# Kernel tuning notes

Measured on AMD Instinct MI355X. Metric: run time of the kernel, lower is better.

The kernel has to match this reference:

```python
import jax, jax.numpy as jnp
import numpy as np

NUM_TYPES = 4  # unique atom types, e.g. H,C,N,O
N_DESC = 384   # descriptor width (nDescriptors())


def setup_inputs() -> dict:
    key = jax.random.key(0)
    k1, k2, k3 = jax.random.split(key, 3)
    n_confs, n_atoms = 2048, 64
    coords = jax.random.normal(k1, (n_confs, n_atoms, 3), dtype=jnp.float32)
    atom_types = jax.random.randint(k2, (n_confs, n_atoms), 0, NUM_TYPES, dtype=jnp.int64)
    W = jax.random.normal(k3, (3, N_DESC), dtype=jnp.float32)
    return {"coords": coords, "atom_types": atom_types, "W": W}


def reference(coords, atom_types, W):
    n_confs, n_atoms, _ = coords.shape
    # stub descriptor computer: per-atom descriptor, (n_confs*n_atoms, N_DESC)
    desc = jnp.tanh(coords.reshape(-1, 3) @ W)
    at2type = atom_types.reshape(-1)                      # (N,)
    # conformer index for every atom: [0,0,...,0,1,1,...]
    at2conf = jnp.repeat(jnp.arange(n_confs, dtype=jnp.int64), n_atoms)
    # stable sort by atom type (routing permutation)
    perm = jnp.argsort(at2type, stable=True)              # (N,)
    desc_sorted = desc[perm]                              # gather (N, N_DESC)
    at2conf_sorted = at2conf[perm]                        # (N,)
    at_type_count = jnp.bincount(at2type, length=NUM_TYPES)  # split sizes per type
    # per-type buckets = desc_sorted split at cumsum(at_type_count); returned
    # concatenated with counts to keep shapes static under jit.
    return desc_sorted, at2conf_sorted, at_type_count
```

## Files before the change

kernel.cpp:

```cpp
#include <hip/hip_runtime.h>

#define NDESC 384
#define NTYPES 4
#define BLOCK_ATOMS 256
#define NTHREADS 384

typedef unsigned int uint32;
typedef unsigned long long u64;
typedef float f4 __attribute__((ext_vector_type(4)));

__device__ __forceinline__ float fast_tanh(float x) {
  float e = __builtin_amdgcn_exp2f(x * 2.8853900817779268f);
  return 1.0f - 2.0f * __builtin_amdgcn_rcpf(1.0f + e);
}

__global__ __launch_bounds__(BLOCK_ATOMS) void hist_kernel(
    const int* __restrict__ types, uint32* __restrict__ blockHist, int n) {
  __shared__ uint32 waveCnt[BLOCK_ATOMS / 64][NTYPES];
  int tid = threadIdx.x;
  int idx = blockIdx.x * BLOCK_ATOMS + tid;
  int ty = (idx < n) ? types[idx] : -1;
  int wave = tid >> 6, lane = tid & 63;
  for (int t = 0; t < NTYPES; ++t) {
    u64 m = __ballot(ty == t);
    if (lane == 0) waveCnt[wave][t] = (uint32)__popcll(m);
  }
  __syncthreads();
  if (tid < NTYPES) {
    uint32 s = 0;
    for (int w = 0; w < BLOCK_ATOMS / 64; ++w) s += waveCnt[w][tid];
    blockHist[blockIdx.x * NTYPES + tid] = s;
  }
}

__global__ __launch_bounds__(NTHREADS, 6) void main_kernel(
    const float* __restrict__ coords, const int* __restrict__ types,
    const float* __restrict__ W, const uint32* __restrict__ blockHist,
    float* __restrict__ descOut, float* __restrict__ confOut,
    float* __restrict__ countsOut, int n, int nb) {
  __shared__ float sC[BLOCK_ATOMS][3];
  __shared__ f4 sRankData[BLOCK_ATOMS];
  __shared__ uint32 waveCnt[BLOCK_ATOMS / 64][NTYPES];
  __shared__ uint32 sTot[NTYPES];
  __shared__ uint32 sOff[NTYPES];
  __shared__ uint32 sCum[NTYPES];

  int tid = threadIdx.x;
  int bid = blockIdx.x;
  int base = bid * BLOCK_ATOMS;

  int r = tid / 96;
  int c = tid - r * 96;
  int d0 = 4 * c;

  f4 W0 = *reinterpret_cast<const f4*>(W + d0);
  f4 W1 = *reinterpret_cast<const f4*>(W + NDESC + d0);
  f4 W2 = *reinterpret_cast<const f4*>(W + 2 * NDESC + d0);

  for (int i = tid; i < BLOCK_ATOMS * 3; i += NTHREADS) {
    int g = base * 3 + i;
    sC[i / 3][i % 3] = (g < n * 3) ? coords[g] : 0.0f;
  }

  int idx = base + tid;
  int ty = -1;
  if (tid < BLOCK_ATOMS && idx < n) ty = types[idx];
  int wave = tid >> 6, lane = tid & 63;
  int myrank = 0;
  if (tid < BLOCK_ATOMS) {
    for (int t = 0; t < NTYPES; ++t) {
      u64 m = __ballot(ty == t);
      if (lane == 0) waveCnt[wave][t] = (uint32)__popcll(m);
      if (t == ty) myrank = (int)__popcll(m & ((1ull << lane) - 1ull));
    }
  }

  if (wave < NTYPES) {
    int t = wave;
    uint32 tot = 0, pre = 0;
    for (int b = lane; b < nb; b += 64) {
      uint32 h = blockHist[b * NTYPES + t];
      tot += h;
      if (b < bid) pre += h;
    }
    for (int off = 32; off > 0; off >>= 1) {
      tot += __shfl_down(tot, off);
      pre += __shfl_down(pre, off);
    }
    if (lane == 0) { sTot[t] = tot; sOff[t] = pre; }
  }
  __syncthreads();
  if (tid == 0) {
    uint32 b = 0, cc = 0;
    for (int t = 0; t < NTYPES; ++t) {
      sOff[t] += b;
      b += sTot[t];
      uint32 cnt = 0;
      for (int w = 0; w < BLOCK_ATOMS / 64; ++w) cnt += waveCnt[w][t];
      sCum[t] = cc;
      cc += cnt;
    }
  }
  if (bid == 0 && tid < NTYPES) countsOut[tid] = (float)sTot[tid];
  __syncthreads();

  if (tid < BLOCK_ATOMS && ty >= 0) {
    uint32 fullrank = (uint32)myrank;
    for (int w = 0; w < wave; ++w) fullrank += waveCnt[w][ty];
    uint32 pos = sOff[ty] + fullrank;
    uint32 brk = sCum[ty] + fullrank;
    f4 rd;
    rd.x = sC[tid][0];
    rd.y = sC[tid][1];
    rd.z = sC[tid][2];
    rd.w = __uint_as_float(pos);
    sRankData[brk] = rd;
    confOut[pos] = (float)(idx >> 6);
  }
  __syncthreads();

  int valid = n - base;
  if (valid > BLOCK_ATOMS) valid = BLOCK_ATOMS;

  if (valid == BLOCK_ATOMS) {
#pragma unroll 4
    for (int k0 = 0; k0 < BLOCK_ATOMS; k0 += 4) {
      int k = k0 + r;
      f4 rd = sRankData[k];
      uint32 pos = __float_as_uint(rd.w);
      f4 v;
      v.x = fast_tanh(rd.x * W0.x + rd.y * W1.x + rd.z * W2.x);
      v.y = fast_tanh(rd.x * W0.y + rd.y * W1.y + rd.z * W2.y);
      v.z = fast_tanh(rd.x * W0.z + rd.y * W1.z + rd.z * W2.z);
      v.w = fast_tanh(rd.x * W0.w + rd.y * W1.w + rd.z * W2.w);
      *reinterpret_cast<f4*>(descOut + (size_t)pos * NDESC + d0) = v;
    }
  } else {
    for (int k0 = 0; k0 < BLOCK_ATOMS; k0 += 4) {
      int k = k0 + r;
      if (k < valid) {
        f4 rd = sRankData[k];
        uint32 pos = __float_as_uint(rd.w);
        f4 v;
        v.x = fast_tanh(rd.x * W0.x + rd.y * W1.x + rd.z * W2.x);
        v.y = fast_tanh(rd.x * W0.y + rd.y * W1.y + rd.z * W2.y);
        v.z = fast_tanh(rd.x * W0.z + rd.y * W1.z + rd.z * W2.z);
        v.w = fast_tanh(rd.x * W0.w + rd.y * W1.w + rd.z * W2.w);
        *reinterpret_cast<f4*>(descOut + (size_t)pos * NDESC + d0) = v;
      }
    }
  }
}

extern "C" void kernel_launch(void* const* d_in, const int* in_sizes, int n_in,
                              void* d_out, int out_size, void* d_ws, size_t ws_size,
                              hipStream_t stream) {
  const float* coords = (const float*)d_in[0];
  const int* types = (const int*)d_in[1];
  const float* W = (const float*)d_in[2];

  int n = in_sizes[1];
  int nb = (n + BLOCK_ATOMS - 1) / BLOCK_ATOMS;

  uint32* blockHist = (uint32*)d_ws;

  float* descOut = (float*)d_out;
  float* confOut = descOut + (size_t)n * NDESC;
  float* countsOut = confOut + n;

  hipLaunchKernelGGL(hist_kernel, dim3(nb), dim3(BLOCK_ATOMS), 0, stream,
                     types, blockHist, n);
  hipLaunchKernelGGL(main_kernel, dim3(nb), dim3(NTHREADS), 0, stream,
                     coords, types, W, blockHist, descOut, confOut, countsOut,
                     n, nb);
}
```

Measured before the change: 46.10 us.

## Split main kernel into producer and store warps with double-buffered LDS tiles

Raises the block to 512 threads. 384 producer threads compute the tanh descriptors for 16-row tiles into a double-buffered shared-memory tile. The other 128 threads stream the previous tile out to the scattered global rows. The intent is to overlap compute with global stores. In exchange it adds a barrier per tile, 48KB of extra LDS and lower occupancy, and only 128 threads now issue all the stores.

```diff
diff --git a/kernel.cpp b/kernel.cpp
--- a/kernel.cpp
+++ b/kernel.cpp
@@ -3,7 +3,11 @@
 #define NDESC 384
 #define NTYPES 4
 #define BLOCK_ATOMS 256
-#define NTHREADS 384
+#define NTHREADS 512
+#define NPROD 384
+#define TILE_ROWS 16
+#define NTILES (BLOCK_ATOMS / TILE_ROWS)
+#define TILE_F4 (TILE_ROWS * NDESC / 4)
 
 typedef unsigned int uint32;
 typedef unsigned long long u64;
@@ -33,11 +37,12 @@
   }
 }
 
-__global__ __launch_bounds__(NTHREADS, 6) void main_kernel(
+__global__ __launch_bounds__(NTHREADS, 4) void main_kernel(
     const float* __restrict__ coords, const int* __restrict__ types,
     const float* __restrict__ W, const uint32* __restrict__ blockHist,
     float* __restrict__ descOut, float* __restrict__ confOut,
     float* __restrict__ countsOut, int n, int nb) {
+  __shared__ f4 tileBuf[2][TILE_F4];
   __shared__ float sC[BLOCK_ATOMS][3];
   __shared__ f4 sRankData[BLOCK_ATOMS];
   __shared__ uint32 waveCnt[BLOCK_ATOMS / 64][NTYPES];
@@ -49,13 +54,11 @@
   int bid = blockIdx.x;
   int base = bid * BLOCK_ATOMS;
 
-  int r = tid / 96;
-  int c = tid - r * 96;
-  int d0 = 4 * c;
-
-  f4 W0 = *reinterpret_cast<const f4*>(W + d0);
-  f4 W1 = *reinterpret_cast<const f4*>(W + NDESC + d0);
-  f4 W2 = *reinterpret_cast<const f4*>(W + 2 * NDESC + d0);
+  int ct = tid % 96;
+  int d0p = 4 * ct;
+  f4 W0 = *reinterpret_cast<const f4*>(W + d0p);
+  f4 W1 = *reinterpret_cast<const f4*>(W + NDESC + d0p);
+  f4 W2 = *reinterpret_cast<const f4*>(W + 2 * NDESC + d0p);
 
   for (int i = tid; i < BLOCK_ATOMS * 3; i += NTHREADS) {
     int g = base * 3 + i;
@@ -123,30 +126,69 @@
   if (valid > BLOCK_ATOMS) valid = BLOCK_ATOMS;
 
   if (valid == BLOCK_ATOMS) {
-#pragma unroll 4
-    for (int k0 = 0; k0 < BLOCK_ATOMS; k0 += 4) {
-      int k = k0 + r;
-      f4 rd = sRankData[k];
-      uint32 pos = __float_as_uint(rd.w);
-      f4 v;
-      v.x = fast_tanh(rd.x * W0.x + rd.y * W1.x + rd.z * W2.x);
-      v.y = fast_tanh(rd.x * W0.y + rd.y * W1.y + rd.z * W2.y);
-      v.z = fast_tanh(rd.x * W0.z + rd.y * W1.z + rd.z * W2.z);
-      v.w = fast_tanh(rd.x * W0.w + rd.y * W1.w + rd.z * W2.w);
-      *reinterpret_cast<f4*>(descOut + (size_t)pos * NDESC + d0) = v;
-    }
-  } else {
-    for (int k0 = 0; k0 < BLOCK_ATOMS; k0 += 4) {
-      int k = k0 + r;
-      if (k < valid) {
-        f4 rd = sRankData[k];
-        uint32 pos = __float_as_uint(rd.w);
+    bool producer = (tid < NPROD);
+    int rbase = tid / 96;
+
+    if (producer) {
+#pragma unroll
+      for (int k = 0; k < 4; ++k) {
+        int rrow = rbase + k * 4;
+        f4 rd = sRankData[rrow];
         f4 v;
         v.x = fast_tanh(rd.x * W0.x + rd.y * W1.x + rd.z * W2.x);
         v.y = fast_tanh(rd.x * W0.y + rd.y * W1.y + rd.z * W2.y);
         v.z = fast_tanh(rd.x * W0.z + rd.y * W1.z + rd.z * W2.z);
         v.w = fast_tanh(rd.x * W0.w + rd.y * W1.w + rd.z * W2.w);
-        *reinterpret_cast<f4*>(descOut + (size_t)pos * NDESC + d0) = v;
+        tileBuf[0][k * NPROD + tid] = v;
+      }
+    }
+    __syncthreads();
+
+    for (int tl = 0; tl < NTILES; ++tl) {
+      int cur = tl & 1;
+      if (producer) {
+        if (tl + 1 < NTILES) {
+          int tbase = (tl + 1) * TILE_ROWS;
+#pragma unroll
+          for (int k = 0; k < 4; ++k) {
+            int rrow = tbase + rbase + k * 4;
+            f4 rd = sRankData[rrow];
+            f4 v;
+            v.x = fast_tanh(rd.x * W0.x + rd.y * W1.x + rd.z * W2.x);
+            v.y = fast_tanh(rd.x * W0.y + rd.y * W1.y + rd.z * W2.y);
+            v.z = fast_tanh(rd.x * W0.z + rd.y * W1.z + rd.z * W2.z);
+            v.w = fast_tanh(rd.x * W0.w + rd.y * W1.w + rd.z * W2.w);
+            tileBuf[cur ^ 1][k * NPROD + tid] = v;
+          }
+        }
+      } else {
+        int u = tid - NPROD;
+#pragma unroll
+        for (int k = 0; k < 12; ++k) {
+          int j = k * 128 + u;
+          int rr = j / 96;
+          int col = j - rr * 96;
+          uint32 pos = __float_as_uint(sRankData[tl * TILE_ROWS + rr].w);
+          f4 v = tileBuf[cur][j];
+          *reinterpret_cast<f4*>(descOut + (size_t)pos * NDESC + 4 * col) = v;
+        }
+      }
+      __syncthreads();
+    }
+  } else {
+    if (tid < NPROD) {
+      for (int k0 = 0; k0 < BLOCK_ATOMS; k0 += 4) {
+        int k = k0 + tid / 96;
+        if (k < valid) {
+          f4 rd = sRankData[k];
+          uint32 pos = __float_as_uint(rd.w);
+          f4 v;
+          v.x = fast_tanh(rd.x * W0.x + rd.y * W1.x + rd.z * W2.x);
+          v.y = fast_tanh(rd.x * W0.y + rd.y * W1.y + rd.z * W2.y);
+          v.z = fast_tanh(rd.x * W0.z + rd.y * W1.z + rd.z * W2.z);
+          v.w = fast_tanh(rd.x * W0.w + rd.y * W1.w + rd.z * W2.w);
+          *reinterpret_cast<f4*>(descOut + (size_t)pos * NDESC + d0p) = v;
+        }
       }
     }
   }
```

After: 45.60 us. About the same (-1.1%).
